# Kernel optimization log

Measured on AMD Instinct MI355X. Metric: run time of the kernel, lower is better.

The kernel has to match this reference:

```python
import math
import jax, jax.numpy as jnp
import numpy as np

B, T, C = 4, 2048, 1024
N_HEAD = 16
HEAD_DIM = C // N_HEAD


def setup_inputs() -> dict:
    key = jax.random.key(0)
    k1, k2, k3, k4, k5 = jax.random.split(key, 5)
    s = 1.0 / math.sqrt(C)
    return {
        "x": jax.random.normal(k1, (B, T, C), dtype=jnp.float32),
        "w_qkv": jax.random.normal(k2, (C, 3 * C), dtype=jnp.float32) * s,
        "b_qkv": jax.random.normal(k3, (3 * C,), dtype=jnp.float32) * 0.01,
        "w_proj": jax.random.normal(k4, (C, C), dtype=jnp.float32) * s,
        "b_proj": jax.random.normal(k5, (C,), dtype=jnp.float32) * 0.01,
    }


def reference(x, w_qkv, b_qkv, w_proj, b_proj):
    Bb, Tt, Cc = x.shape
    qkv = x @ w_qkv + b_qkv  # [B, T, 3C]
    q, k, v = jnp.split(qkv, 3, axis=-1)
    # [B, H, T, D]
    q = q.reshape(Bb, Tt, N_HEAD, HEAD_DIM).transpose(0, 2, 1, 3)
    k = k.reshape(Bb, Tt, N_HEAD, HEAD_DIM).transpose(0, 2, 1, 3)
    v = v.reshape(Bb, Tt, N_HEAD, HEAD_DIM).transpose(0, 2, 1, 3)
    scale = 1.0 / math.sqrt(HEAD_DIM)
    att = jnp.einsum('bhqd,bhkd->bhqk', q, k) * scale  # [B, H, T, T]
    causal = jnp.tril(jnp.ones((Tt, Tt), dtype=bool))
    att = jnp.where(causal[None, None, :, :], att, -jnp.inf)
    att = jax.nn.softmax(att, axis=-1)
    y = jnp.einsum('bhqk,bhkd->bhqd', att, v)  # [B, H, T, D]
    y = y.transpose(0, 2, 1, 3).reshape(Bb, Tt, Cc)
    return y @ w_proj + b_proj
```

## Files before the change

### kernel.cpp

```cpp
#include <hip/hip_runtime.h>
#include <hip/hip_bf16.h>

#define B_   4
#define T_   2048
#define C_   1024
#define NH   16
#define HD   64

typedef unsigned short u16;
typedef short bf16x8 __attribute__((ext_vector_type(8)));
typedef short bf16x4 __attribute__((ext_vector_type(4)));
typedef float f32x4  __attribute__((ext_vector_type(4)));

#define MFMA_BF16(a, b, c) __builtin_amdgcn_mfma_f32_16x16x32_bf16((a), (b), (c), 0, 0, 0)

__device__ __forceinline__ u16 f2bf(float f) {
    unsigned u = __float_as_uint(f);
    return (u16)((u + 0x7FFFu + ((u >> 16) & 1u)) >> 16);
}
__device__ __forceinline__ bf16x8 pack8(float4 f0, float4 f1) {
    bf16x8 r;
    r[0] = (short)f2bf(f0.x); r[1] = (short)f2bf(f0.y);
    r[2] = (short)f2bf(f0.z); r[3] = (short)f2bf(f0.w);
    r[4] = (short)f2bf(f1.x); r[5] = (short)f2bf(f1.y);
    r[6] = (short)f2bf(f1.z); r[7] = (short)f2bf(f1.w);
    return r;
}
__device__ __forceinline__ bf16x4 pack4(f32x4 v) {
    bf16x4 r;
    r[0] = (short)f2bf(v[0]); r[1] = (short)f2bf(v[1]);
    r[2] = (short)f2bf(v[2]); r[3] = (short)f2bf(v[3]);
    return r;
}

__device__ __forceinline__ void gl2lds16(const void* g, void* l) {
    __builtin_amdgcn_global_load_lds(
        (const __attribute__((address_space(1))) void*)g,
        (__attribute__((address_space(3))) void*)l,
        16, 0, 0);
}

__global__ __launch_bounds__(256) void cast_x(
    const float* __restrict__ x, u16* __restrict__ xb)
{
    int i = (blockIdx.x * 256 + threadIdx.x) * 8;
    float4 f0 = *reinterpret_cast<const float4*>(&x[i]);
    float4 f1 = *reinterpret_cast<const float4*>(&x[i + 4]);
    *reinterpret_cast<bf16x8*>(&xb[i]) = pack8(f0, f1);
}

__global__ __launch_bounds__(256) void transpose_w(
    const float* __restrict__ src, u16* __restrict__ dst, int R, int Ccols)
{
    __shared__ float tile[32][33];
    const int c0 = blockIdx.x * 32, r0 = blockIdx.y * 32;
    const int tx = threadIdx.x, ty = threadIdx.y;
#pragma unroll
    for (int i = 0; i < 4; ++i)
        tile[ty + 8 * i][tx] = src[(size_t)(r0 + ty + 8 * i) * Ccols + c0 + tx];
    __syncthreads();
#pragma unroll
    for (int i = 0; i < 4; ++i)
        dst[(size_t)(c0 + ty + 8 * i) * R + r0 + tx] = f2bf(tile[tx][ty + 8 * i]);
}

__global__ __launch_bounds__(256, 3) void qkv_gemm_mfma(
    const u16* __restrict__ xb, const u16* __restrict__ wqT,
    const float* __restrict__ bqkv,
    u16* __restrict__ Qo, u16* __restrict__ Ko, u16* __restrict__ Vo)
{
    __shared__ __attribute__((aligned(16))) u16 As[128 * 32];
    __shared__ __attribute__((aligned(16))) u16 Bs[128 * 32];

    const int t = threadIdx.x, lane = t & 63, w = t >> 6;
    const int n = lane & 15, quad = lane >> 4;
    const int wr = w >> 1, wc = w & 1;
    const int m0 = blockIdx.y * 128, n0 = blockIdx.x * 128;
    const int tmask = t & ~63;

    f32x4 acc[4][4] = {};

    for (int k0 = 0; k0 < 1024; k0 += 32) {
        __syncthreads();
#pragma unroll
        for (int p = 0; p < 2; ++p) {
            int id = t + p * 256;
            int row = id >> 2, c = (id & 3) ^ (row & 3);
            gl2lds16(&xb[(size_t)(m0 + row) * 1024 + k0 + c * 8], &As[(tmask + p * 256) * 8]);
            gl2lds16(&wqT[(size_t)(n0 + row) * 1024 + k0 + c * 8], &Bs[(tmask + p * 256) * 8]);
        }
        __syncthreads();

        const int slot = (quad ^ (n & 3)) * 8;
        bf16x8 a[4], b[4];
#pragma unroll
        for (int i = 0; i < 4; ++i)
            a[i] = *reinterpret_cast<const bf16x8*>(&As[(wr * 64 + i * 16 + n) * 32 + slot]);
#pragma unroll
        for (int j = 0; j < 4; ++j)
            b[j] = *reinterpret_cast<const bf16x8*>(&Bs[(wc * 64 + j * 16 + n) * 32 + slot]);
#pragma unroll
        for (int i = 0; i < 4; ++i)
#pragma unroll
            for (int j = 0; j < 4; ++j)
                acc[i][j] = MFMA_BF16(a[i], b[j], acc[i][j]);
    }

    const int colbase = n0 + wc * 64;
    const int which = colbase >> 10;
    const int h = (colbase & 1023) >> 6;
    u16* dst = (which == 0) ? Qo : ((which == 1) ? Ko : Vo);
    const float sc = (which == 0) ? 0.125f : 1.0f;
#pragma unroll
    for (int i = 0; i < 4; ++i) {
#pragma unroll
        for (int r = 0; r < 4; ++r) {
            int m = m0 + wr * 64 + i * 16 + quad * 4 + r;
            int bb = m >> 11, trow = m & 2047;
            size_t obase = (((size_t)(bb * NH + h)) * 2048 + trow) * 64;
#pragma unroll
            for (int j = 0; j < 4; ++j) {
                float v = acc[i][j][r] + bqkv[colbase + j * 16 + n];
                dst[obase + j * 16 + n] = f2bf(v * sc);
            }
        }
    }
}

__global__ __launch_bounds__(256) void transpose_v(
    const u16* __restrict__ V, u16* __restrict__ Vt)
{
    __shared__ u16 tile[64 * 82];
    const int bh = blockIdx.y, t0 = blockIdx.x * 64;
    const int t = threadIdx.x;
    const u16* src = V + (size_t)bh * 131072 + (size_t)t0 * 64;
    u16* dst = Vt + (size_t)bh * 131072 + t0;
#pragma unroll
    for (int p = 0; p < 2; ++p) {
        int id = t + p * 256;
        int row = id >> 3, seg = id & 7;
        ushort4 u0 = *reinterpret_cast<const ushort4*>(&src[row * 64 + seg * 8]);
        ushort4 u1 = *reinterpret_cast<const ushort4*>(&src[row * 64 + seg * 8 + 4]);
        u16* tp = &tile[row * 82 + seg * 8];
        tp[0] = u0.x; tp[1] = u0.y; tp[2] = u0.z; tp[3] = u0.w;
        tp[4] = u1.x; tp[5] = u1.y; tp[6] = u1.z; tp[7] = u1.w;
    }
    __syncthreads();
#pragma unroll
    for (int p = 0; p < 2; ++p) {
        int id = t + p * 256;
        int d = id >> 3, ks = id & 7;
        u16 u[8];
#pragma unroll
        for (int j = 0; j < 8; ++j) u[j] = tile[(ks * 8 + j) * 82 + d];
        *reinterpret_cast<ushort4*>(&dst[(size_t)d * 2048 + ks * 8])     = make_ushort4(u[0], u[1], u[2], u[3]);
        *reinterpret_cast<ushort4*>(&dst[(size_t)d * 2048 + ks * 8 + 4]) = make_ushort4(u[4], u[5], u[6], u[7]);
    }
}

__global__ __launch_bounds__(256, 2) void attn_mfma(
    const u16* __restrict__ Q, const u16* __restrict__ K,
    const u16* __restrict__ Vt, u16* __restrict__ Y)
{
    const int pairi = blockIdx.x;
    const int bh = blockIdx.y;
    const int b = bh >> 4, h = bh & 15;
    const size_t base = (size_t)bh * (T_ * HD);

    __shared__ __attribute__((aligned(16))) u16 QPs[128 * 64];
    __shared__ __attribute__((aligned(16))) u16 Ks[128 * 64];
    __shared__ __attribute__((aligned(16))) u16 Vs[64 * 128];

    const int t = threadIdx.x, lane = t & 63, w = t >> 6;
    const int n = lane & 15, quad = lane >> 4;
    const int tmask = t & ~63;

    for (int ph = 0; ph < 2; ++ph) {
        const int qt = ph ? pairi : 15 - pairi;
        const int q0 = qt * 128;
        const int qw_lo = q0 + w * 32;
        const int qw_hi = qw_lo + 31;

        __syncthreads();

#pragma unroll
        for (int p = 0; p < 4; ++p) {
            int id = t + p * 256;
            int row = id >> 3, c = (id & 7) ^ (row & 7);
            gl2lds16(&Q[base + (size_t)(q0 + row) * 64 + c * 8], &QPs[(tmask + p * 256) * 8]);
        }

        f32x4 o[2][4] = {};
        float mst[2] = {-1e30f, -1e30f}, lst[2] = {0.f, 0.f};
        bf16x8 qa[2][2];

        const int nst = qt + 1;
        for (int st = 0; st < nst; ++st) {
            const int k0 = st * 128;
            __syncthreads();
#pragma unroll
            for (int p = 0; p < 4; ++p) {
                int id = t + p * 256;
                int row = id >> 3, c = (id & 7) ^ (row & 7);
                gl2lds16(&K[base + (size_t)(k0 + row) * 64 + c * 8], &Ks[(tmask + p * 256) * 8]);
            }
#pragma unroll
            for (int p = 0; p < 4; ++p) {
                int id = t + p * 256;
                int row = id >> 4, cs = id & 15, c = cs ^ (row & 7);
                gl2lds16(&Vt[base + (size_t)row * 2048 + k0 + c * 8], &Vs[(tmask + p * 256) * 8]);
            }
            __syncthreads();

            if (st == 0) {
#pragma unroll
                for (int nt2 = 0; nt2 < 2; ++nt2)
#pragma unroll
                    for (int dh = 0; dh < 2; ++dh) {
                        int row = w * 32 + nt2 * 16 + n;
                        int slot = (quad + dh * 4) ^ (n & 7);
                        qa[nt2][dh] = *reinterpret_cast<const bf16x8*>(&QPs[row * 64 + slot * 8]);
                    }
            }

#pragma unroll
            for (int sub = 0; sub < 2; ++sub) {
                const int k0s = k0 + sub * 64;
                if (k0s > qw_hi) continue;
                const u16* Kc = &Ks[sub * 64 * 64];

                bf16x8 kf[4][2];
#pragma unroll
                for (int mt = 0; mt < 4; ++mt)
#pragma unroll
                    for (int dh = 0; dh < 2; ++dh) {
                        int row = mt * 16 + n;
                        int slot = (quad + dh * 4) ^ (n & 7);
                        kf[mt][dh] = *reinterpret_cast<const bf16x8*>(&Kc[row * 64 + slot * 8]);
                    }
                f32x4 s2[2][4] = {};
#pragma unroll
                for (int nt2 = 0; nt2 < 2; ++nt2)
#pragma unroll
                    for (int mt = 0; mt < 4; ++mt)
#pragma unroll
                        for (int dh = 0; dh < 2; ++dh)
                            s2[nt2][mt] = MFMA_BF16(kf[mt][dh], qa[nt2][dh], s2[nt2][mt]);

                if (k0s + 63 > qw_lo) {
#pragma unroll
                    for (int nt2 = 0; nt2 < 2; ++nt2) {
                        int qrel = (qw_lo + nt2 * 16 + n) - k0s;
#pragma unroll
                        for (int mt = 0; mt < 4; ++mt)
#pragma unroll
                            for (int r = 0; r < 4; ++r)
                                if (mt * 16 + quad * 4 + r > qrel) s2[nt2][mt][r] = -1e30f;
                    }
                }

                float alpha[2];
#pragma unroll
                for (int nt2 = 0; nt2 < 2; ++nt2) {
                    float mx = -1e30f;
#pragma unroll
                    for (int mt = 0; mt < 4; ++mt)
                        mx = fmaxf(mx, fmaxf(fmaxf(s2[nt2][mt][0], s2[nt2][mt][1]),
                                             fmaxf(s2[nt2][mt][2], s2[nt2][mt][3])));
                    mx = fmaxf(mx, __shfl_xor(mx, 16, 64));
                    mx = fmaxf(mx, __shfl_xor(mx, 32, 64));
                    float mnew = fmaxf(mst[nt2], mx);
                    alpha[nt2] = __expf(mst[nt2] - mnew);
                    float rs = 0.f;
#pragma unroll
                    for (int mt = 0; mt < 4; ++mt)
#pragma unroll
                        for (int r = 0; r < 4; ++r) {
                            float p = __expf(s2[nt2][mt][r] - mnew);
                            s2[nt2][mt][r] = p;
                            rs += p;
                        }
                    rs += __shfl_xor(rs, 16, 64);
                    rs += __shfl_xor(rs, 32, 64);
                    lst[nt2] = lst[nt2] * alpha[nt2] + rs;
                    mst[nt2] = mnew;
                }

#pragma unroll
                for (int nt2 = 0; nt2 < 2; ++nt2)
#pragma unroll
                    for (int mt = 0; mt < 4; ++mt) {
                        int kc = mt * 2 + (quad >> 1);
                        int off = (w * 32 + nt2 * 16 + n) * 64 + (kc ^ (n & 7)) * 8 + (quad & 1) * 4;
                        *reinterpret_cast<bf16x4*>(&QPs[off]) = pack4(s2[nt2][mt]);
                    }

#pragma unroll
                for (int nt2 = 0; nt2 < 2; ++nt2)
#pragma unroll
                    for (int dt = 0; dt < 4; ++dt)
                        o[nt2][dt] *= alpha[nt2];

                bf16x8 pf[2][2];
#pragma unroll
                for (int nt2 = 0; nt2 < 2; ++nt2)
#pragma unroll
                    for (int kh = 0; kh < 2; ++kh) {
                        int kc = kh * 4 + quad;
                        int off = (w * 32 + nt2 * 16 + n) * 64 + (kc ^ (n & 7)) * 8;
                        pf[nt2][kh] = *reinterpret_cast<const bf16x8*>(&QPs[off]);
                    }
                bf16x8 vf[4][2];
#pragma unroll
                for (int dt = 0; dt < 4; ++dt)
#pragma unroll
                    for (int kh = 0; kh < 2; ++kh) {
                        int row = dt * 16 + n;
                        int slot = ((sub * 8 + kh * 4 + quad) ^ (n & 7));
                        vf[dt][kh] = *reinterpret_cast<const bf16x8*>(&Vs[row * 128 + slot * 8]);
                    }
#pragma unroll
                for (int nt2 = 0; nt2 < 2; ++nt2)
#pragma unroll
                    for (int dt = 0; dt < 4; ++dt)
#pragma unroll
                        for (int kh = 0; kh < 2; ++kh)
                            o[nt2][dt] = MFMA_BF16(vf[dt][kh], pf[nt2][kh], o[nt2][dt]);
            }
        }

#pragma unroll
        for (int nt2 = 0; nt2 < 2; ++nt2) {
            float inv = 1.f / lst[nt2];
            int qg = qw_lo + nt2 * 16 + n;
            size_t ob = (((size_t)(b * 2048 + qg)) * NH + h) * 64;
#pragma unroll
            for (int dt = 0; dt < 4; ++dt) {
                ushort4 stv = make_ushort4(f2bf(o[nt2][dt][0] * inv), f2bf(o[nt2][dt][1] * inv),
                                           f2bf(o[nt2][dt][2] * inv), f2bf(o[nt2][dt][3] * inv));
                *reinterpret_cast<ushort4*>(&Y[ob + dt * 16 + quad * 4]) = stv;
            }
        }
    }
}

__global__ __launch_bounds__(256, 3) void proj_gemm_mfma(
    const u16* __restrict__ A, const u16* __restrict__ BT,
    const float* __restrict__ bias, float* __restrict__ out)
{
    __shared__ __attribute__((aligned(16))) u16 As[128 * 32];
    __shared__ __attribute__((aligned(16))) u16 Bs[128 * 32];

    const int t = threadIdx.x, lane = t & 63, w = t >> 6;
    const int n = lane & 15, quad = lane >> 4;
    const int wr = w >> 1, wc = w & 1;
    const int m0 = blockIdx.y * 128, n0 = blockIdx.x * 128;
    const int tmask = t & ~63;

    f32x4 acc[4][4] = {};

    for (int k0 = 0; k0 < 1024; k0 += 32) {
        __syncthreads();
#pragma unroll
        for (int p = 0; p < 2; ++p) {
            int id = t + p * 256;
            int row = id >> 2, c = (id & 3) ^ (row & 3);
            gl2lds16(&A[(size_t)(m0 + row) * 1024 + k0 + c * 8], &As[(tmask + p * 256) * 8]);
            gl2lds16(&BT[(size_t)(n0 + row) * 1024 + k0 + c * 8], &Bs[(tmask + p * 256) * 8]);
        }
        __syncthreads();

        const int slot = (quad ^ (n & 3)) * 8;
        bf16x8 a[4], b[4];
#pragma unroll
        for (int i = 0; i < 4; ++i)
            a[i] = *reinterpret_cast<const bf16x8*>(&As[(wr * 64 + i * 16 + n) * 32 + slot]);
#pragma unroll
        for (int j = 0; j < 4; ++j)
            b[j] = *reinterpret_cast<const bf16x8*>(&Bs[(wc * 64 + j * 16 + n) * 32 + slot]);
#pragma unroll
        for (int i = 0; i < 4; ++i)
#pragma unroll
            for (int j = 0; j < 4; ++j)
                acc[i][j] = MFMA_BF16(a[i], b[j], acc[i][j]);
    }

#pragma unroll
    for (int i = 0; i < 4; ++i)
#pragma unroll
        for (int r = 0; r < 4; ++r) {
            int m = m0 + wr * 64 + i * 16 + quad * 4 + r;
#pragma unroll
            for (int j = 0; j < 4; ++j) {
                int col = n0 + wc * 64 + j * 16 + n;
                out[(size_t)m * 1024 + col] = acc[i][j][r] + bias[col];
            }
        }
}

extern "C" void kernel_launch(void* const* d_in, const int* in_sizes, int n_in,
                              void* d_out, int out_size, void* d_ws, size_t ws_size,
                              hipStream_t stream) {
    const float* x      = (const float*)d_in[0];
    const float* w_qkv  = (const float*)d_in[1];
    const float* b_qkv  = (const float*)d_in[2];
    const float* w_proj = (const float*)d_in[3];
    const float* b_proj = (const float*)d_in[4];
    float* out = (float*)d_out;

    const size_t E16 = 8388608;
    u16* ws  = (u16*)d_ws;
    u16* Qp  = ws;
    u16* Kp  = ws + E16;
    u16* Vp  = ws + 2 * E16;
    u16* wqT = ws + 3 * E16;
    u16* VtP = ws + 3 * E16;
    u16* Yp  = ws + 2 * E16;
    u16* wpT = ws;
    u16* xb  = (u16*)d_out;

    cast_x<<<dim3(4096), 256, 0, stream>>>(x, xb);
    transpose_w<<<dim3(96, 32), dim3(32, 8), 0, stream>>>(w_qkv, wqT, 1024, 3072);
    qkv_gemm_mfma<<<dim3(24, 64), 256, 0, stream>>>(xb, wqT, b_qkv, Qp, Kp, Vp);
    transpose_v<<<dim3(32, 64), 256, 0, stream>>>(Vp, VtP);
    attn_mfma<<<dim3(8, 64), 256, 0, stream>>>(Qp, Kp, VtP, Yp);
    transpose_w<<<dim3(32, 32), dim3(32, 8), 0, stream>>>(w_proj, wpT, 1024, 1024);
    proj_gemm_mfma<<<dim3(8, 64), 256, 0, stream>>>(Yp, wpT, b_proj, out);
}
```

Baseline: 279.2 us.

## Fuse V transpose into QKV GEMM epilogue and use exp2 softmax

The QKV GEMM epilogue now writes V directly in transposed [B,H,D,T] layout using packed bf16x4 stores, which removes the separate transpose_v kernel launch and its extra pass over V. The Q scale folds in log2(e), so attention can use exp2f in place of __expf. The bf16 packing helpers switch to the hardware paired float2-to-bf16 conversion. Workspace aliasing is rearranged so Y no longer overlaps the transposed V buffer. The V stores are strided by T per d-row and may coalesce less well than before.

Measured after the change: 291.1 us. +4.3%, slower.

```diff
diff --git a/kernel.cpp b/kernel.cpp
--- a/kernel.cpp
+++ b/kernel.cpp
@@ -18,19 +18,19 @@
     unsigned u = __float_as_uint(f);
     return (u16)((u + 0x7FFFu + ((u >> 16) & 1u)) >> 16);
 }
+__device__ __forceinline__ unsigned pk2(float a, float b) {
+    float2 f; f.x = a; f.y = b;
+    __hip_bfloat162 h = __float22bfloat162_rn(f);
+    unsigned u; __builtin_memcpy(&u, &h, 4); return u;
+}
+__device__ __forceinline__ bf16x4 pack4(f32x4 v) {
+    uint2 u; u.x = pk2(v[0], v[1]); u.y = pk2(v[2], v[3]);
+    bf16x4 r; __builtin_memcpy(&r, &u, 8); return r;
+}
 __device__ __forceinline__ bf16x8 pack8(float4 f0, float4 f1) {
-    bf16x8 r;
-    r[0] = (short)f2bf(f0.x); r[1] = (short)f2bf(f0.y);
-    r[2] = (short)f2bf(f0.z); r[3] = (short)f2bf(f0.w);
-    r[4] = (short)f2bf(f1.x); r[5] = (short)f2bf(f1.y);
-    r[6] = (short)f2bf(f1.z); r[7] = (short)f2bf(f1.w);
-    return r;
-}
-__device__ __forceinline__ bf16x4 pack4(f32x4 v) {
-    bf16x4 r;
-    r[0] = (short)f2bf(v[0]); r[1] = (short)f2bf(v[1]);
-    r[2] = (short)f2bf(v[2]); r[3] = (short)f2bf(v[3]);
-    return r;
+    uint4 u; u.x = pk2(f0.x, f0.y); u.y = pk2(f0.z, f0.w);
+    u.z = pk2(f1.x, f1.y); u.w = pk2(f1.z, f1.w);
+    bf16x8 r; __builtin_memcpy(&r, &u, 16); return r;
 }
 
 __device__ __forceinline__ void gl2lds16(const void* g, void* l) {
@@ -67,7 +67,7 @@
 __global__ __launch_bounds__(256, 3) void qkv_gemm_mfma(
     const u16* __restrict__ xb, const u16* __restrict__ wqT,
     const float* __restrict__ bqkv,
-    u16* __restrict__ Qo, u16* __restrict__ Ko, u16* __restrict__ Vo)
+    u16* __restrict__ Qo, u16* __restrict__ Ko, u16* __restrict__ Vt)
 {
     __shared__ __attribute__((aligned(16))) u16 As[128 * 32];
     __shared__ __attribute__((aligned(16))) u16 Bs[128 * 32];
@@ -108,53 +108,39 @@
 
     const int colbase = n0 + wc * 64;
     const int which = colbase >> 10;
-    const int h = (colbase & 1023) >> 6;
-    u16* dst = (which == 0) ? Qo : ((which == 1) ? Ko : Vo);
-    const float sc = (which == 0) ? 0.125f : 1.0f;
-#pragma unroll
-    for (int i = 0; i < 4; ++i) {
-#pragma unroll
-        for (int r = 0; r < 4; ++r) {
-            int m = m0 + wr * 64 + i * 16 + quad * 4 + r;
-            int bb = m >> 11, trow = m & 2047;
-            size_t obase = (((size_t)(bb * NH + h)) * 2048 + trow) * 64;
+    const int bb = m0 >> 11, t0 = m0 & 2047;
+
+    if (which == 2) {
+        const int hh = (colbase & 1023) >> 6;
+        u16* dstv = Vt + ((size_t)(bb * NH + hh)) * (HD * T_);
+#pragma unroll
+        for (int i = 0; i < 4; ++i) {
+            int tt = t0 + wr * 64 + i * 16 + quad * 4;
 #pragma unroll
             for (int j = 0; j < 4; ++j) {
-                float v = acc[i][j][r] + bqkv[colbase + j * 16 + n];
-                dst[obase + j * 16 + n] = f2bf(v * sc);
-            }
-        }
-    }
-}
-
-__global__ __launch_bounds__(256) void transpose_v(
-    const u16* __restrict__ V, u16* __restrict__ Vt)
-{
-    __shared__ u16 tile[64 * 82];
-    const int bh = blockIdx.y, t0 = blockIdx.x * 64;
-    const int t = threadIdx.x;
-    const u16* src = V + (size_t)bh * 131072 + (size_t)t0 * 64;
-    u16* dst = Vt + (size_t)bh * 131072 + t0;
-#pragma unroll
-    for (int p = 0; p < 2; ++p) {
-        int id = t + p * 256;
-        int row = id >> 3, seg = id & 7;
-        ushort4 u0 = *reinterpret_cast<const ushort4*>(&src[row * 64 + seg * 8]);
-        ushort4 u1 = *reinterpret_cast<const ushort4*>(&src[row * 64 + seg * 8 + 4]);
-        u16* tp = &tile[row * 82 + seg * 8];
-        tp[0] = u0.x; tp[1] = u0.y; tp[2] = u0.z; tp[3] = u0.w;
-        tp[4] = u1.x; tp[5] = u1.y; tp[6] = u1.z; tp[7] = u1.w;
-    }
-    __syncthreads();
-#pragma unroll
-    for (int p = 0; p < 2; ++p) {
-        int id = t + p * 256;
-        int d = id >> 3, ks = id & 7;
-        u16 u[8];
-#pragma unroll
-        for (int j = 0; j < 8; ++j) u[j] = tile[(ks * 8 + j) * 82 + d];
-        *reinterpret_cast<ushort4*>(&dst[(size_t)d * 2048 + ks * 8])     = make_ushort4(u[0], u[1], u[2], u[3]);
-        *reinterpret_cast<ushort4*>(&dst[(size_t)d * 2048 + ks * 8 + 4]) = make_ushort4(u[4], u[5], u[6], u[7]);
+                float bv = bqkv[colbase + j * 16 + n];
+                f32x4 vv = acc[i][j] + bv;
+                int d = j * 16 + n;
+                *reinterpret_cast<bf16x4*>(&dstv[(size_t)d * T_ + tt]) = pack4(vv);
+            }
+        }
+    } else {
+        const int h = (colbase & 1023) >> 6;
+        u16* dst = (which == 0) ? Qo : Ko;
+        const float sc = (which == 0) ? 0.125f * 1.44269504088896f : 1.0f;
+#pragma unroll
+        for (int i = 0; i < 4; ++i) {
+#pragma unroll
+            for (int r = 0; r < 4; ++r) {
+                int trow = t0 + wr * 64 + i * 16 + quad * 4 + r;
+                size_t obase = (((size_t)(bb * NH + h)) * 2048 + trow) * 64;
+#pragma unroll
+                for (int j = 0; j < 4; ++j) {
+                    float v = (acc[i][j][r] + bqkv[colbase + j * 16 + n]) * sc;
+                    dst[obase + j * 16 + n] = f2bf(v);
+                }
+            }
+        }
     }
 }
 
@@ -270,13 +256,13 @@
                     mx = fmaxf(mx, __shfl_xor(mx, 16, 64));
                     mx = fmaxf(mx, __shfl_xor(mx, 32, 64));
                     float mnew = fmaxf(mst[nt2], mx);
-                    alpha[nt2] = __expf(mst[nt2] - mnew);
+                    alpha[nt2] = exp2f(mst[nt2] - mnew);
                     float rs = 0.f;
 #pragma unroll
                     for (int mt = 0; mt < 4; ++mt)
 #pragma unroll
                         for (int r = 0; r < 4; ++r) {
-                            float p = __expf(s2[nt2][mt][r] - mnew);
+                            float p = exp2f(s2[nt2][mt][r] - mnew);
                             s2[nt2][mt][r] = p;
                             rs += p;
                         }
@@ -335,11 +321,8 @@
             int qg = qw_lo + nt2 * 16 + n;
             size_t ob = (((size_t)(b * 2048 + qg)) * NH + h) * 64;
 #pragma unroll
-            for (int dt = 0; dt < 4; ++dt) {
-                ushort4 stv = make_ushort4(f2bf(o[nt2][dt][0] * inv), f2bf(o[nt2][dt][1] * inv),
-                                           f2bf(o[nt2][dt][2] * inv), f2bf(o[nt2][dt][3] * inv));
-                *reinterpret_cast<ushort4*>(&Y[ob + dt * 16 + quad * 4]) = stv;
-            }
+            for (int dt = 0; dt < 4; ++dt)
+                *reinterpret_cast<bf16x4*>(&Y[ob + dt * 16 + quad * 4]) = pack4(o[nt2][dt] * inv);
         }
     }
 }
@@ -412,17 +395,15 @@
     u16* ws  = (u16*)d_ws;
     u16* Qp  = ws;
     u16* Kp  = ws + E16;
-    u16* Vp  = ws + 2 * E16;
+    u16* VtP = ws + 2 * E16;
     u16* wqT = ws + 3 * E16;
-    u16* VtP = ws + 3 * E16;
-    u16* Yp  = ws + 2 * E16;
+    u16* Yp  = ws + 3 * E16;
     u16* wpT = ws;
     u16* xb  = (u16*)d_out;
 
     cast_x<<<dim3(4096), 256, 0, stream>>>(x, xb);
     transpose_w<<<dim3(96, 32), dim3(32, 8), 0, stream>>>(w_qkv, wqT, 1024, 3072);
-    qkv_gemm_mfma<<<dim3(24, 64), 256, 0, stream>>>(xb, wqT, b_qkv, Qp, Kp, Vp);
-    transpose_v<<<dim3(32, 64), 256, 0, stream>>>(Vp, VtP);
+    qkv_gemm_mfma<<<dim3(24, 64), 256, 0, stream>>>(xb, wqT, b_qkv, Qp, Kp, VtP);
     attn_mfma<<<dim3(8, 64), 256, 0, stream>>>(Qp, Kp, VtP, Yp);
     transpose_w<<<dim3(32, 32), dim3(32, 8), 0, stream>>>(w_proj, wpT, 1024, 1024);
     proj_gemm_mfma<<<dim3(8, 64), 256, 0, stream>>>(Yp, wpT, b_proj, out);
```
